# Kernel optimization log

Measured on AMD Instinct MI355X. Metric: run time of the kernel, lower is better.

## Reference

```python
import jax, jax.numpy as jnp
import numpy as np

B, H, N, Dh = 4, 16, 8192, 64
EPS = 1e-5          # masked-fill epsilon for D
CLAMP_EPS = 1e-10   # clamp_abs epsilon for gamma denominator
PROJ_EPS = 4e-3     # geoopt float32 projection epsilon


def _sumsq(x):
    return jnp.sum(x * x, axis=-1, keepdims=True)


def _pt0back(x, v, k):
    # geoopt parallel_transport0back: transport v from x back to origin
    # = v * lambda_x / lambda_0 = v / (1 + k ||x||^2)
    return v / jnp.maximum(1.0 + k * _sumsq(x), 1e-15)


def _lambda_x(x, k):
    # conformal factor 2 / (1 + k ||x||^2)
    return 2.0 / jnp.maximum(1.0 + k * _sumsq(x), 1e-15)


def _clamp_abs(x, eps):
    s = jnp.where(x >= 0, 1.0, -1.0)
    return s * jnp.maximum(jnp.abs(x), eps)


def _project(x, k):
    # clip points to the ball of radius (1-eps)/sqrt(|k|) when k < 0
    maxnorm = jnp.where(k < 0, (1.0 - PROJ_EPS) / jnp.sqrt(jnp.abs(k) + 1e-15), 1e15)
    norm = jnp.maximum(jnp.linalg.norm(x, axis=-1, keepdims=True), 1e-15)
    return jnp.where(norm > maxnorm, x / norm * maxnorm, x)


def _artan_k(u, k):
    sk = jnp.sqrt(jnp.abs(k) + 1e-15)
    su = sk * u
    hyp = jnp.arctanh(jnp.clip(su, -1.0 + 1e-7, 1.0 - 1e-7))
    return jnp.where(k < 0, hyp, jnp.arctan(su)) / sk


def _tan_k(u, k):
    sk = jnp.sqrt(jnp.abs(k) + 1e-15)
    su = sk * u
    return jnp.where(k < 0, jnp.tanh(su), jnp.tan(su)) / sk


def _mobius_scalar_mul(r, x, k):
    xnorm = jnp.maximum(jnp.linalg.norm(x, axis=-1, keepdims=True), 1e-15)
    return _tan_k(r * _artan_k(xnorm, k), k) * x / xnorm


def setup_inputs() -> dict:
    key = jax.random.key(0)
    kq, kk, kv = jax.random.split(key, 3)
    Q = 0.5 * jax.random.normal(kq, (B, H, N, Dh), dtype=jnp.float32)
    K = 0.5 * jax.random.normal(kk, (B, H, N, Dh), dtype=jnp.float32)
    # scale V so points lie well inside the Poincare ball: ||V||^2 ~ 0.16 < 1/|k|
    V = 0.05 * jax.random.normal(kv, (B, H, N, Dh), dtype=jnp.float32)
    mask = jnp.ones((N,), dtype=jnp.float32)
    curvatures = jnp.linspace(-2.0, -0.5, H, dtype=jnp.float32).reshape(H, 1, 1)
    return {"Q": Q, "K": K, "V": V, "mask": mask, "curvatures": curvatures}


def reference(Q, K, V, mask, curvatures):
    k = curvatures                      # [H,1,1], broadcasts over [B,H,N,1]
    m = mask[None, :, None]             # [1,N,1] -> broadcasts over [B,H,N,D]
    v1 = _pt0back(V, Q, k)              # transport Q from V back to origin
    v2 = _pt0back(V, K, k)
    gamma = _lambda_x(V, k)             # [B,H,N,1]
    denom = _clamp_abs(gamma - 1.0, CLAMP_EPS)
    x = gamma / denom * V * m           # [B,H,N,D]
    v1 = jax.nn.elu(v1) + 1.0           # positive feature map
    v2 = denom * (jax.nn.elu(v2) + 1.0) * m
    v2_sum = jnp.sum(v2, axis=-2)       # [B,H,D]
    Dn = jnp.einsum('bhnd,bhd->bhn', v1, v2_sum)
    D_inv = 1.0 / jnp.where(Dn == 0, EPS, Dn)
    context = jnp.einsum('bhnd,bhne->bhde', v2, x)          # [B,H,D,D]
    X = jnp.einsum('bhde,bhnd,bhn->bhne', context, v1, D_inv)
    X = _project(X, k)
    X = _mobius_scalar_mul(0.5, X, k)
    X = _project(X, k)
    return X
```

## Files before the change

### kernel.cpp

```cpp
#include <hip/hip_runtime.h>
#include <math.h>

#define NROWS   8192
#define DHH     64
#define BHCOUNT 64
#define HCOUNT  16
#define SPLITA  16
#define CHUNKA  (NROWS / SPLITA)
#define GA      32
#define LSTR    68
#define SPLITB  32
#define CHUNKB  (NROWS / SPLITB)
#define CTXSZ   4160
#define EPS_DN  1e-5f
#define PROJ_EPS 0.004f
#define NGA     (CHUNKA / GA)
#define ABUF    (2 * GA * LSTR)

__device__ __forceinline__ float elu1(float x) {
    return x > 0.0f ? x + 1.0f : expf(x);
}
__device__ __forceinline__ float rlane(float v, int l) {
    return __uint_as_float(__builtin_amdgcn_readlane(__float_as_uint(v), l));
}

__global__ __launch_bounds__(256, 4) void phaseA(
        const float* __restrict__ Kp, const float* __restrict__ Vp,
        const float* __restrict__ maskp, const float* __restrict__ curvp,
        float* __restrict__ denomWs, float* __restrict__ partials) {
    __shared__ __align__(16) float smem[2 * ABUF];
    const int bx = blockIdx.x;
    const int bh = bx / SPLITA, sp = bx % SPLITA;
    const float k = curvp[bh % HCOUNT];
    const int t = threadIdx.x;
    const int rowBase = sp * CHUNKA;
    const float* Kb = Kp + (size_t)bh * NROWS * DHH;
    const float* Vb = Vp + (size_t)bh * NROWS * DHH;

    const int wave = t >> 6;
    const int lane = t & 63;
    const int d0 = (lane >> 3) * 8;
    const int e0 = (lane & 7) * 8;
    const int rloc = t >> 4;
    const int c4   = t & 15;

    float acc[8][8];
    #pragma unroll
    for (int i = 0; i < 8; ++i)
        #pragma unroll
        for (int j = 0; j < 8; ++j) acc[i][j] = 0.f;
    float4 v2sum4 = make_float4(0.f, 0.f, 0.f, 0.f);

    float4 pV[2], pK[2];
    #pragma unroll
    for (int pass = 0; pass < 2; ++pass) {
        const int n = rowBase + pass * 16 + rloc;
        pV[pass] = *(const float4*)(Vb + (size_t)n * DHH + 4 * c4);
        pK[pass] = *(const float4*)(Kb + (size_t)n * DHH + 4 * c4);
    }

    for (int g = 0; g < NGA; ++g) {
        float4 nV[2], nK[2];
        if (g + 1 < NGA) {
            #pragma unroll
            for (int pass = 0; pass < 2; ++pass) {
                const int n = rowBase + (g + 1) * GA + pass * 16 + rloc;
                nV[pass] = *(const float4*)(Vb + (size_t)n * DHH + 4 * c4);
                nK[pass] = *(const float4*)(Kb + (size_t)n * DHH + 4 * c4);
            }
        }
        float* v2s = smem + (g & 1) * ABUF;
        float* xs  = v2s + GA * LSTR;
        #pragma unroll
        for (int pass = 0; pass < 2; ++pass) {
            const int rl = pass * 16 + rloc;
            const int n = rowBase + g * GA + rl;
            const float4 v4 = pV[pass];
            const float4 k4 = pK[pass];
            float ss = v4.x*v4.x + v4.y*v4.y + v4.z*v4.z + v4.w*v4.w;
            ss += __shfl_xor(ss, 1);
            ss += __shfl_xor(ss, 2);
            ss += __shfl_xor(ss, 4);
            ss += __shfl_xor(ss, 8);
            const float dv    = fmaxf(1.0f + k * ss, 1e-15f);
            const float gamma = 2.0f / dv;
            const float gm1   = gamma - 1.0f;
            const float dnm   = (gm1 >= 0.0f ? 1.0f : -1.0f) * fmaxf(fabsf(gm1), 1e-10f);
            const float m     = maskp[n];
            const float idv   = 1.0f / dv;
            const float cv2   = dnm * m;
            const float cx    = (gamma / dnm) * m;
            float4 v2v, xv;
            v2v.x = cv2 * elu1(k4.x * idv);
            v2v.y = cv2 * elu1(k4.y * idv);
            v2v.z = cv2 * elu1(k4.z * idv);
            v2v.w = cv2 * elu1(k4.w * idv);
            xv.x = cx * v4.x; xv.y = cx * v4.y; xv.z = cx * v4.z; xv.w = cx * v4.w;
            *(float4*)&v2s[rl * LSTR + 4 * c4] = v2v;
            *(float4*)&xs [rl * LSTR + 4 * c4] = xv;
            v2sum4.x += v2v.x; v2sum4.y += v2v.y; v2sum4.z += v2v.z; v2sum4.w += v2v.w;
            if (c4 == 0) denomWs[(size_t)bh * NROWS + n] = dv;
        }
        __syncthreads();
        #pragma unroll 2
        for (int r = wave; r < GA; r += 4) {
            const float4 alo = *(const float4*)&v2s[r * LSTR + d0];
            const float4 ahi = *(const float4*)&v2s[r * LSTR + d0 + 4];
            const float4 blo = *(const float4*)&xs [r * LSTR + e0];
            const float4 bhi = *(const float4*)&xs [r * LSTR + e0 + 4];
            const float af[8] = {alo.x, alo.y, alo.z, alo.w, ahi.x, ahi.y, ahi.z, ahi.w};
            const float bf[8] = {blo.x, blo.y, blo.z, blo.w, bhi.x, bhi.y, bhi.z, bhi.w};
            #pragma unroll
            for (int i = 0; i < 8; ++i)
                #pragma unroll
                for (int j = 0; j < 8; ++j)
                    acc[i][j] += af[i] * bf[j];
        }
        pV[0] = nV[0]; pV[1] = nV[1]; pK[0] = nK[0]; pK[1] = nK[1];
    }
    __syncthreads();

    float* red = smem;
    for (int w = 0; w < 4; ++w) {
        if (wave == w) {
            #pragma unroll
            for (int i = 0; i < 8; ++i) {
                const int base = (d0 + i) * DHH + e0;
                float4 lo = make_float4(acc[i][0], acc[i][1], acc[i][2], acc[i][3]);
                float4 hi = make_float4(acc[i][4], acc[i][5], acc[i][6], acc[i][7]);
                if (w != 0) {
                    const float4 plo = *(const float4*)&red[base];
                    const float4 phi = *(const float4*)&red[base + 4];
                    lo.x += plo.x; lo.y += plo.y; lo.z += plo.z; lo.w += plo.w;
                    hi.x += phi.x; hi.y += phi.y; hi.z += phi.z; hi.w += phi.w;
                }
                *(float4*)&red[base]     = lo;
                *(float4*)&red[base + 4] = hi;
            }
        }
        __syncthreads();
    }

    float* pbase = partials + (size_t)(bh * SPLITA + sp) * CTXSZ;
    #pragma unroll
    for (int i = 0; i < 4; ++i) {
        const int idx = t * 16 + i * 4;
        *(float4*)(pbase + idx) = *(const float4*)&red[idx];
    }
    __syncthreads();
    *(float4*)&smem[t * 4] = v2sum4;
    __syncthreads();
    if (t < DHH) {
        const int cc = t >> 2, j = t & 3;
        float s = 0.f;
        #pragma unroll
        for (int q = 0; q < 16; ++q) s += smem[(q * 16 + cc) * 4 + j];
        pbase[4096 + t] = s;
    }
}

#define RSEG 16
__global__ __launch_bounds__(256) void reduceCtx(
        const float* __restrict__ partials, float* __restrict__ ctxsum) {
    const int bh  = blockIdx.x / RSEG;
    const int seg = blockIdx.x % RSEG;
    const int t = threadIdx.x;
    const int base = seg * 260;
    for (int i = t; i < 260; i += 256) {
        const int idx = base + i;
        const float* p = partials + (size_t)bh * SPLITA * CTXSZ + idx;
        float s = 0.f;
        #pragma unroll
        for (int sp = 0; sp < SPLITA; ++sp) s += p[(size_t)sp * CTXSZ];
        ctxsum[(size_t)bh * CTXSZ + idx] = s;
    }
}

__global__ __launch_bounds__(256, 4) void phaseB(
        const float* __restrict__ Qp, const float* __restrict__ curvp,
        const float* __restrict__ denomWs, const float* __restrict__ ctxsum,
        float* __restrict__ outp) {
    const int bx = blockIdx.x;
    const int bh = bx / SPLITB, sp = bx % SPLITB;
    const float k = curvp[bh % HCOUNT];
    const float sk = sqrtf(fabsf(k) + 1e-15f);
    const float maxnorm = (k < 0.0f) ? (1.0f - PROJ_EPS) / sk : 1e15f;
    const int t = threadIdx.x;
    const int wave = t >> 6;
    const int lane = t & 63;

    const float* cb = ctxsum + (size_t)bh * CTXSZ;
    float ctxr[DHH];
    #pragma unroll
    for (int d = 0; d < DHH; ++d) ctxr[d] = cb[d * DHH + lane];
    const float v2s = cb[4096 + lane];

    const float* Qb  = Qp   + (size_t)bh * NROWS * DHH;
    float*       Ob  = outp + (size_t)bh * NROWS * DHH;
    const float* dvb = denomWs + (size_t)bh * NROWS;
    const int n0 = sp * CHUNKB + wave * 64;
    const int lm = lane & 3;

    float qc0 = Qb[(size_t)(n0 + 0) * DHH + lane];
    float qc1 = Qb[(size_t)(n0 + 1) * DHH + lane];
    float qc2 = Qb[(size_t)(n0 + 2) * DHH + lane];
    float qc3 = Qb[(size_t)(n0 + 3) * DHH + lane];
    float dc0 = dvb[n0 + 0], dc1 = dvb[n0 + 1], dc2 = dvb[n0 + 2], dc3 = dvb[n0 + 3];

    #pragma unroll 1
    for (int g = 0; g < 16; ++g) {
        const int nb = n0 + g * 4;
        float qn0, qn1, qn2, qn3, dn0, dn1, dn2, dn3;
        if (g < 15) {
            qn0 = Qb[(size_t)(nb + 4) * DHH + lane];
            qn1 = Qb[(size_t)(nb + 5) * DHH + lane];
            qn2 = Qb[(size_t)(nb + 6) * DHH + lane];
            qn3 = Qb[(size_t)(nb + 7) * DHH + lane];
            dn0 = dvb[nb + 4]; dn1 = dvb[nb + 5]; dn2 = dvb[nb + 6]; dn3 = dvb[nb + 7];
        }
        const float v10 = elu1(qc0 * (1.0f / dc0));
        const float v11 = elu1(qc1 * (1.0f / dc1));
        const float v12 = elu1(qc2 * (1.0f / dc2));
        const float v13 = elu1(qc3 * (1.0f / dc3));
        float t0 = v10 * v2s, t1 = v11 * v2s, t2 = v12 * v2s, t3 = v13 * v2s;
        t0 += __shfl_xor(t0, 1); t1 += __shfl_xor(t1, 1);
        t2 += __shfl_xor(t2, 1); t3 += __shfl_xor(t3, 1);
        t0 += __shfl_xor(t0, 2); t1 += __shfl_xor(t1, 2);
        t2 += __shfl_xor(t2, 2); t3 += __shfl_xor(t3, 2);
        float p = (lm == 0) ? t0 : (lm == 1) ? t1 : (lm == 2) ? t2 : t3;
        p += __shfl_xor(p, 4); p += __shfl_xor(p, 8);
        p += __shfl_xor(p, 16); p += __shfl_xor(p, 32);
        p = (p == 0.0f) ? EPS_DN : p;
        const float pinv = 1.0f / p;
        const float di0 = rlane(pinv, 0), di1 = rlane(pinv, 1);
        const float di2 = rlane(pinv, 2), di3 = rlane(pinv, 3);
        float a0 = 0.f, a1 = 0.f, a2 = 0.f, a3 = 0.f;
        #pragma unroll
        for (int d = 0; d < DHH; ++d) {
            a0 = fmaf(rlane(v10, d), ctxr[d], a0);
            a1 = fmaf(rlane(v11, d), ctxr[d], a1);
            a2 = fmaf(rlane(v12, d), ctxr[d], a2);
            a3 = fmaf(rlane(v13, d), ctxr[d], a3);
        }
        a0 *= di0; a1 *= di1; a2 *= di2; a3 *= di3;
        float u0 = a0 * a0, u1 = a1 * a1, u2 = a2 * a2, u3 = a3 * a3;
        u0 += __shfl_xor(u0, 1); u1 += __shfl_xor(u1, 1);
        u2 += __shfl_xor(u2, 1); u3 += __shfl_xor(u3, 1);
        u0 += __shfl_xor(u0, 2); u1 += __shfl_xor(u1, 2);
        u2 += __shfl_xor(u2, 2); u3 += __shfl_xor(u3, 2);
        float s = (lm == 0) ? u0 : (lm == 1) ? u1 : (lm == 2) ? u2 : u3;
        s += __shfl_xor(s, 4); s += __shfl_xor(s, 8);
        s += __shfl_xor(s, 16); s += __shfl_xor(s, 32);
        const float norm = fmaxf(sqrtf(s), 1e-15f);
        const float f1 = (norm > maxnorm) ? (maxnorm / norm) : 1.0f;
        const float xnorm = fmaxf(norm * f1, 1e-15f);
        const float su = sk * xnorm;
        float tk;
        if (k < 0.0f) {
            const float suc = fminf(su, 1.0f - 1e-7f);
            tk = suc / (1.0f + sqrtf(fmaxf(1.0f - suc * suc, 0.0f)));
        } else {
            tk = su / (1.0f + sqrtf(1.0f + su * su));
        }
        tk /= sk;
        const float f2 = tk / xnorm;
        const float n3 = fmaxf(fabsf(tk), 1e-15f);
        const float f3 = (n3 > maxnorm) ? (maxnorm / n3) : 1.0f;
        const float fac = f1 * f2 * f3;
        const float f0_ = rlane(fac, 0), f1_ = rlane(fac, 1);
        const float f2_ = rlane(fac, 2), f3_ = rlane(fac, 3);
        Ob[(size_t)(nb + 0) * DHH + lane] = a0 * f0_;
        Ob[(size_t)(nb + 1) * DHH + lane] = a1 * f1_;
        Ob[(size_t)(nb + 2) * DHH + lane] = a2 * f2_;
        Ob[(size_t)(nb + 3) * DHH + lane] = a3 * f3_;
        qc0 = qn0; qc1 = qn1; qc2 = qn2; qc3 = qn3;
        dc0 = dn0; dc1 = dn1; dc2 = dn2; dc3 = dn3;
    }
}

extern "C" void kernel_launch(void* const* d_in, const int* in_sizes, int n_in,
                              void* d_out, int out_size, void* d_ws, size_t ws_size,
                              hipStream_t stream) {
    const float* Q    = (const float*)d_in[0];
    const float* K    = (const float*)d_in[1];
    const float* V    = (const float*)d_in[2];
    const float* mask = (const float*)d_in[3];
    const float* curv = (const float*)d_in[4];
    float* out = (float*)d_out;

    float* denomWs  = (float*)d_ws;
    float* partials = denomWs + (size_t)BHCOUNT * NROWS;
    float* ctxsum   = partials + (size_t)BHCOUNT * SPLITA * CTXSZ;

    phaseA<<<dim3(BHCOUNT * SPLITA), dim3(256), 0, stream>>>(K, V, mask, curv, denomWs, partials);
    reduceCtx<<<dim3(BHCOUNT * RSEG), dim3(256), 0, stream>>>(partials, ctxsum);
    phaseB<<<dim3(BHCOUNT * SPLITB), dim3(256), 0, stream>>>(Q, curv, denomWs, ctxsum, out);
}
```

Measured before the change: 578.2 us.

## Rewrite phaseB as LDS-tiled 8x8 register-blocked matmul with swizzled transposed features

phaseB now stages the context matrix and v2 sum in shared memory and computes each wave's 64x64 output tile as an 8x8-per-lane outer-product GEMM. Previously each output row was formed with per-lane readlane broadcasts. The transformed Q features are written transposed into a per-wave LDS buffer with an XOR swizzle, which is meant to avoid bank conflicts. Row norms are reduced over 8 lanes, and outputs are stored as float4. The min-occupancy hint on launch_bounds is removed from both kernels, so the compiler may use more registers (acc[64]) at the cost of occupancy.

```diff
diff --git a/kernel.cpp b/kernel.cpp
--- a/kernel.cpp
+++ b/kernel.cpp
@@ -20,11 +20,8 @@
 __device__ __forceinline__ float elu1(float x) {
     return x > 0.0f ? x + 1.0f : expf(x);
 }
-__device__ __forceinline__ float rlane(float v, int l) {
-    return __uint_as_float(__builtin_amdgcn_readlane(__float_as_uint(v), l));
-}
-
-__global__ __launch_bounds__(256, 4) void phaseA(
+
+__global__ __launch_bounds__(256) void phaseA(
         const float* __restrict__ Kp, const float* __restrict__ Vp,
         const float* __restrict__ maskp, const float* __restrict__ curvp,
         float* __restrict__ denomWs, float* __restrict__ partials) {
@@ -176,10 +173,15 @@
     }
 }
 
-__global__ __launch_bounds__(256, 4) void phaseB(
+__global__ __launch_bounds__(256) void phaseB(
         const float* __restrict__ Qp, const float* __restrict__ curvp,
         const float* __restrict__ denomWs, const float* __restrict__ ctxsum,
         float* __restrict__ outp) {
+    __shared__ __align__(16) float ctx[DHH * DHH];
+    __shared__ __align__(16) float v2sum_l[DHH];
+    __shared__ __align__(16) float v1T[4][32 * 64];
+    __shared__ float dnW[4][64];
+
     const int bx = blockIdx.x;
     const int bh = bx / SPLITB, sp = bx % SPLITB;
     const float k = curvp[bh % HCOUNT];
@@ -190,68 +192,95 @@
     const int lane = t & 63;
 
     const float* cb = ctxsum + (size_t)bh * CTXSZ;
-    float ctxr[DHH];
-    #pragma unroll
-    for (int d = 0; d < DHH; ++d) ctxr[d] = cb[d * DHH + lane];
-    const float v2s = cb[4096 + lane];
+    #pragma unroll
+    for (int i = 0; i < 16; ++i) {
+        const int idx = i * 256 + t;
+        ctx[idx] = cb[idx];
+    }
+    if (t < DHH) v2sum_l[t] = cb[4096 + t];
+    __syncthreads();
 
     const float* Qb  = Qp   + (size_t)bh * NROWS * DHH;
     float*       Ob  = outp + (size_t)bh * NROWS * DHH;
     const float* dvb = denomWs + (size_t)bh * NROWS;
+
+    const int r8 = lane >> 3;
+    const int c8 = lane & 7;
+    const int a0 = r8 * 8;
+    const int e0 = c8 * 8;
     const int n0 = sp * CHUNKB + wave * 64;
-    const int lm = lane & 3;
-
-    float qc0 = Qb[(size_t)(n0 + 0) * DHH + lane];
-    float qc1 = Qb[(size_t)(n0 + 1) * DHH + lane];
-    float qc2 = Qb[(size_t)(n0 + 2) * DHH + lane];
-    float qc3 = Qb[(size_t)(n0 + 3) * DHH + lane];
-    float dc0 = dvb[n0 + 0], dc1 = dvb[n0 + 1], dc2 = dvb[n0 + 2], dc3 = dvb[n0 + 3];
-
-    #pragma unroll 1
-    for (int g = 0; g < 16; ++g) {
-        const int nb = n0 + g * 4;
-        float qn0, qn1, qn2, qn3, dn0, dn1, dn2, dn3;
-        if (g < 15) {
-            qn0 = Qb[(size_t)(nb + 4) * DHH + lane];
-            qn1 = Qb[(size_t)(nb + 5) * DHH + lane];
-            qn2 = Qb[(size_t)(nb + 6) * DHH + lane];
-            qn3 = Qb[(size_t)(nb + 7) * DHH + lane];
-            dn0 = dvb[nb + 4]; dn1 = dvb[nb + 5]; dn2 = dvb[nb + 6]; dn3 = dvb[nb + 7];
-        }
-        const float v10 = elu1(qc0 * (1.0f / dc0));
-        const float v11 = elu1(qc1 * (1.0f / dc1));
-        const float v12 = elu1(qc2 * (1.0f / dc2));
-        const float v13 = elu1(qc3 * (1.0f / dc3));
-        float t0 = v10 * v2s, t1 = v11 * v2s, t2 = v12 * v2s, t3 = v13 * v2s;
-        t0 += __shfl_xor(t0, 1); t1 += __shfl_xor(t1, 1);
-        t2 += __shfl_xor(t2, 1); t3 += __shfl_xor(t3, 1);
-        t0 += __shfl_xor(t0, 2); t1 += __shfl_xor(t1, 2);
-        t2 += __shfl_xor(t2, 2); t3 += __shfl_xor(t3, 2);
-        float p = (lm == 0) ? t0 : (lm == 1) ? t1 : (lm == 2) ? t2 : t3;
-        p += __shfl_xor(p, 4); p += __shfl_xor(p, 8);
-        p += __shfl_xor(p, 16); p += __shfl_xor(p, 32);
-        p = (p == 0.0f) ? EPS_DN : p;
-        const float pinv = 1.0f / p;
-        const float di0 = rlane(pinv, 0), di1 = rlane(pinv, 1);
-        const float di2 = rlane(pinv, 2), di3 = rlane(pinv, 3);
-        float a0 = 0.f, a1 = 0.f, a2 = 0.f, a3 = 0.f;
-        #pragma unroll
-        for (int d = 0; d < DHH; ++d) {
-            a0 = fmaf(rlane(v10, d), ctxr[d], a0);
-            a1 = fmaf(rlane(v11, d), ctxr[d], a1);
-            a2 = fmaf(rlane(v12, d), ctxr[d], a2);
-            a3 = fmaf(rlane(v13, d), ctxr[d], a3);
-        }
-        a0 *= di0; a1 *= di1; a2 *= di2; a3 *= di3;
-        float u0 = a0 * a0, u1 = a1 * a1, u2 = a2 * a2, u3 = a3 * a3;
-        u0 += __shfl_xor(u0, 1); u1 += __shfl_xor(u1, 1);
-        u2 += __shfl_xor(u2, 1); u3 += __shfl_xor(u3, 1);
-        u0 += __shfl_xor(u0, 2); u1 += __shfl_xor(u1, 2);
-        u2 += __shfl_xor(u2, 2); u3 += __shfl_xor(u3, 2);
-        float s = (lm == 0) ? u0 : (lm == 1) ? u1 : (lm == 2) ? u2 : u3;
-        s += __shfl_xor(s, 4); s += __shfl_xor(s, 8);
-        s += __shfl_xor(s, 16); s += __shfl_xor(s, 32);
-        const float norm = fmaxf(sqrtf(s), 1e-15f);
+    float* vT  = &v1T[wave][0];
+    float* dnw = &dnW[wave][0];
+    const int wcolbase = 4 * c8;
+
+    float acc[8][8];
+    #pragma unroll
+    for (int i = 0; i < 8; ++i)
+        #pragma unroll
+        for (int j = 0; j < 8; ++j) acc[i][j] = 0.f;
+
+    #pragma unroll
+    for (int h = 0; h < 2; ++h) {
+        const float4 vs4 = *(const float4*)&v2sum_l[h * 32 + 4 * c8];
+        #pragma unroll
+        for (int p = 0; p < 8; ++p) {
+            const int n = p * 8 + r8;
+            const float4 q4 = *(const float4*)(Qb + (size_t)(n0 + n) * DHH + h * 32 + 4 * c8);
+            const float idv = 1.0f / dvb[n0 + n];
+            float4 v14;
+            v14.x = elu1(q4.x * idv);
+            v14.y = elu1(q4.y * idv);
+            v14.z = elu1(q4.z * idv);
+            v14.w = elu1(q4.w * idv);
+            const int wcol = n ^ wcolbase;
+            vT[(4 * c8 + 0) * 64 + wcol] = v14.x;
+            vT[(4 * c8 + 1) * 64 + wcol] = v14.y;
+            vT[(4 * c8 + 2) * 64 + wcol] = v14.z;
+            vT[(4 * c8 + 3) * 64 + wcol] = v14.w;
+            float dnp = v14.x * vs4.x + v14.y * vs4.y + v14.z * vs4.z + v14.w * vs4.w;
+            dnp += __shfl_xor(dnp, 1);
+            dnp += __shfl_xor(dnp, 2);
+            dnp += __shfl_xor(dnp, 4);
+            if (c8 == 0) {
+                if (h == 0) dnw[n] = dnp;
+                else        dnw[n] += dnp;
+            }
+        }
+        const float* ctxh = &ctx[h * 32 * 64];
+        #pragma unroll 1
+        for (int dd4 = 0; dd4 < 32; dd4 += 4) {
+            const int vb1 = dd4 * 64 + (a0 ^ dd4);
+            const int vb2 = dd4 * 64 + ((a0 + 4) ^ dd4);
+            #pragma unroll
+            for (int q = 0; q < 4; ++q) {
+                const float4 alo = *(const float4*)&vT[vb1 + q * 64];
+                const float4 ahi = *(const float4*)&vT[vb2 + q * 64];
+                const float4 blo = *(const float4*)&ctxh[(dd4 + q) * 64 + e0];
+                const float4 bhi = *(const float4*)&ctxh[(dd4 + q) * 64 + e0 + 4];
+                const float af[8] = {alo.x, alo.y, alo.z, alo.w, ahi.x, ahi.y, ahi.z, ahi.w};
+                const float bf[8] = {blo.x, blo.y, blo.z, blo.w, bhi.x, bhi.y, bhi.z, bhi.w};
+                #pragma unroll
+                for (int i = 0; i < 8; ++i)
+                    #pragma unroll
+                    for (int j = 0; j < 8; ++j)
+                        acc[i][j] += af[i] * bf[j];
+            }
+        }
+    }
+
+    #pragma unroll
+    for (int i = 0; i < 8; ++i) {
+        float dn = dnw[a0 + i];
+        dn = (dn == 0.0f) ? EPS_DN : dn;
+        const float di = 1.0f / dn;
+        #pragma unroll
+        for (int j = 0; j < 8; ++j) acc[i][j] *= di;
+        float ss = acc[i][0]*acc[i][0] + acc[i][1]*acc[i][1] + acc[i][2]*acc[i][2] + acc[i][3]*acc[i][3]
+                 + acc[i][4]*acc[i][4] + acc[i][5]*acc[i][5] + acc[i][6]*acc[i][6] + acc[i][7]*acc[i][7];
+        ss += __shfl_xor(ss, 1);
+        ss += __shfl_xor(ss, 2);
+        ss += __shfl_xor(ss, 4);
+        const float norm = fmaxf(sqrtf(ss), 1e-15f);
         const float f1 = (norm > maxnorm) ? (maxnorm / norm) : 1.0f;
         const float xnorm = fmaxf(norm * f1, 1e-15f);
         const float su = sk * xnorm;
@@ -267,14 +296,11 @@
         const float n3 = fmaxf(fabsf(tk), 1e-15f);
         const float f3 = (n3 > maxnorm) ? (maxnorm / n3) : 1.0f;
         const float fac = f1 * f2 * f3;
-        const float f0_ = rlane(fac, 0), f1_ = rlane(fac, 1);
-        const float f2_ = rlane(fac, 2), f3_ = rlane(fac, 3);
-        Ob[(size_t)(nb + 0) * DHH + lane] = a0 * f0_;
-        Ob[(size_t)(nb + 1) * DHH + lane] = a1 * f1_;
-        Ob[(size_t)(nb + 2) * DHH + lane] = a2 * f2_;
-        Ob[(size_t)(nb + 3) * DHH + lane] = a3 * f3_;
-        qc0 = qn0; qc1 = qn1; qc2 = qn2; qc3 = qn3;
-        dc0 = dn0; dc1 = dn1; dc2 = dn2; dc3 = dn3;
+        float4 o1 = make_float4(acc[i][0]*fac, acc[i][1]*fac, acc[i][2]*fac, acc[i][3]*fac);
+        float4 o2 = make_float4(acc[i][4]*fac, acc[i][5]*fac, acc[i][6]*fac, acc[i][7]*fac);
+        float* orow = Ob + (size_t)(n0 + a0 + i) * DHH + e0;
+        *(float4*)orow       = o1;
+        *(float4*)(orow + 4) = o2;
     }
 }
 
```

After: 514.3 us. -11.1%, faster.
